# Optimization experiments

Hardware: AMD Instinct MI355X
Metric: run time of the kernel (lower is better)

## Reference

```python
import jax, jax.numpy as jnp
import numpy as np

N = 131072
C = 8
W = 256


def setup_inputs() -> dict:
    key = jax.random.key(0)
    ks = jax.random.split(key, 10)
    s1 = 1.0 / np.sqrt(3.0)
    sw = 1.0 / np.sqrt(W)
    return {
        "positions": jax.random.normal(ks[0], (N, 3), dtype=jnp.float32),
        "times": jax.random.randint(ks[1], (N,), 0, C, dtype=jnp.int64),
        "W1": jax.random.normal(ks[2], (C, 3, W), dtype=jnp.float32) * s1,
        "b1": jnp.zeros((C, W), dtype=jnp.float32),
        "W2": jax.random.normal(ks[3], (C, W, W), dtype=jnp.float32) * sw,
        "b2": jnp.zeros((C, W), dtype=jnp.float32),
        "W3": jax.random.normal(ks[4], (C, W, W), dtype=jnp.float32) * sw,
        "b3": jnp.zeros((C, W), dtype=jnp.float32),
        "W4": jax.random.normal(ks[5], (C, W, 3), dtype=jnp.float32) * sw,
        "b4": jnp.zeros((C, 3), dtype=jnp.float32),
    }


def _mlp(x, w1, c1, w2, c2, w3, c3, w4, c4):
    # 4-layer MLP, Tanh hidden activations and Tanh output activation
    h = jnp.tanh(x @ w1 + c1)
    h = jnp.tanh(h @ w2 + c2)
    h = jnp.tanh(h @ w3 + c3)
    return jnp.tanh(h @ w4 + c4)


def reference(positions, times, W1, b1, W2, b2, W3, b3, W4, b4):
    # offsets = zeros_like(positions); offsets[times==i] = mlp_i(positions[times==i])
    # classes partition the points, so this equals a per-class select-sum.
    offsets = jnp.zeros_like(positions)
    for i in range(C):  # small fixed class count
        out_i = _mlp(positions, W1[i], b1[i], W2[i], b2[i], W3[i], b3[i], W4[i], b4[i])
        mask = (times == i)[:, None]  # [N,1]
        offsets = jnp.where(mask, out_i, offsets)
    return offsets
```

## Files before the change

kernel.cpp:

```cpp
#include <hip/hip_runtime.h>
#include <stdint.h>

#define N_PTS 131072
#define NCLS 8
#define MT 64
#define CAP 32768
#define PS 2.8853900817779268f

typedef __bf16 bf16x8 __attribute__((ext_vector_type(8)));
typedef float f32x4 __attribute__((ext_vector_type(4)));

__device__ __forceinline__ float exp2_fast(float a) {
#if __has_builtin(__builtin_amdgcn_exp2f)
  return __builtin_amdgcn_exp2f(a);
#else
  return exp2f(a);
#endif
}

__device__ __forceinline__ float tanh_p2(float a) {
  return fmaf(-2.0f, __builtin_amdgcn_rcpf(exp2_fast(a) + 1.0f), 1.0f);
}

__device__ __forceinline__ unsigned short f2bf_rne(float f) {
  unsigned u = __float_as_uint(f);
  u = u + 0x7fffu + ((u >> 16) & 1u);
  return (unsigned short)(u >> 16);
}

__device__ __forceinline__ unsigned pack_bf16(float a, float b) {
  unsigned ua = __float_as_uint(a) + 0x8000u;
  unsigned ub = __float_as_uint(b) + 0x8000u;
  return __builtin_amdgcn_perm(ub, ua, 0x07060302u);
}

#define PK2_BLKS 512
#define MISC_BLKS 177
#define MISC_N 45184
#define SCAT_BLKS 512
#define PREP_GRID (PK2_BLKS + MISC_BLKS + SCAT_BLKS)

__global__ __launch_bounds__(256) void k_prep(
    const int* __restrict__ times,
    const float* __restrict__ W1, const float* __restrict__ b1,
    const float* __restrict__ W2, const float* __restrict__ b2,
    const float* __restrict__ W3, const float* __restrict__ b3,
    const float* __restrict__ W4, const float* __restrict__ b4,
    int* __restrict__ hdr, int* __restrict__ sortedIdx,
    unsigned short* __restrict__ packed23,
    float* __restrict__ w1p, float* __restrict__ b2p,
    float* __restrict__ b3p, float* __restrict__ b4p,
    unsigned short* __restrict__ W4p) {
  __shared__ int lh[NCLS], lbase[NCLS];

  int b = blockIdx.x;
  int tid = threadIdx.x;

  if (b < PK2_BLKS) {
    int cl = b >> 5;
    int k8 = b & 31;
    int j = tid;
    int l = cl >> 3, c = cl & 7;
    const float* W = (l ? W3 : W2) + c * 65536 + k8 * 8 * 256 + j;
    float v0 = W[0],        v1 = W[256],     v2 = W[2 * 256], v3 = W[3 * 256];
    float v4 = W[4 * 256],  v5 = W[5 * 256], v6 = W[6 * 256], v7 = W[7 * 256];
    uint4 pk;
    pk.x = (unsigned)f2bf_rne(PS * v0) | ((unsigned)f2bf_rne(PS * v1) << 16);
    pk.y = (unsigned)f2bf_rne(PS * v2) | ((unsigned)f2bf_rne(PS * v3) << 16);
    pk.z = (unsigned)f2bf_rne(PS * v4) | ((unsigned)f2bf_rne(PS * v5) << 16);
    pk.w = (unsigned)f2bf_rne(PS * v6) | ((unsigned)f2bf_rne(PS * v7) << 16);
    *(uint4*)&packed23[cl * 65536 + (k8 * 256 + j) * 8] = pk;
  } else if (b < PK2_BLKS + MISC_BLKS) {
    int e2 = (b - PK2_BLKS) * 256 + tid;
    if (e2 < 8192) {
      int c = e2 >> 10, rem = e2 & 1023;
      int j = rem >> 2, t = rem & 3;
      float v = (t < 3) ? W1[c * 768 + t * 256 + j] : b1[c * 256 + j];
      w1p[e2] = PS * v;
    } else if (e2 < 10240) {
      int i = e2 - 8192;
      b2p[i] = PS * b2[i];
    } else if (e2 < 12288) {
      int i = e2 - 10240;
      b3p[i] = PS * b3[i];
    } else if (e2 < 12416) {
      int i = e2 - 12288;
      int c = i >> 4, r = i & 15;
      b4p[i] = (r < 3) ? PS * b4[c * 3 + r] : 0.0f;
    } else if (e2 < MISC_N) {
      int i = e2 - 12416;
      int c = i >> 12, rem = i & 4095;
      int jj = rem & 7, j = (rem >> 3) & 15, k = ((rem >> 7) << 3) + jj;
      float v = (j < 3) ? PS * W4[c * 768 + k * 3 + j] : 0.0f;
      W4p[c * 4096 + rem] = f2bf_rne(v);
    }
  } else {
    int sb = b - (PK2_BLKS + MISC_BLKS);
    if (tid < NCLS) lh[tid] = 0;
    __syncthreads();
    int i = sb * 256 + tid;
    int t = times[i];
    int r = atomicAdd(&lh[t], 1);
    __syncthreads();
    if (tid < NCLS) lbase[tid] = lh[tid] ? atomicAdd(&hdr[tid], lh[tid]) : 0;
    __syncthreads();
    sortedIdx[t * CAP + lbase[t] + r] = i;
  }
}

template <bool PRELOAD_NEXT>
__device__ __forceinline__ void mfma_layer16(
    unsigned short (*__restrict__ Abuf)[MT][8],
    bf16x8 (&af)[2][8],
    bf16x8 (&afn)[2][8],
    const bf16x8* __restrict__ nextAf,
    const float* __restrict__ biasp,
    int tid) {
  int lane = tid & 63, w = tid >> 6;
  int quad = lane >> 4, l16 = lane & 15;
  int jcol = w * 32 + l16;

  f32x4 acc[2][4];
#pragma unroll
  for (int jf = 0; jf < 2; jf++) {
    f32x4 bv = *(const f32x4*)&biasp[w * 32 + jf * 16 + quad * 4];
#pragma unroll
    for (int mt = 0; mt < 4; mt++) acc[jf][mt] = bv;
  }

#pragma unroll
  for (int kb = 0; kb < 8; kb++) {
    int kq = kb * 4 + quad;
    bf16x8 bfr[4];
#pragma unroll
    for (int mt = 0; mt < 4; mt++)
      bfr[mt] = *(const bf16x8*)&Abuf[kq][mt * 16 + l16][0];
#pragma unroll
    for (int jf = 0; jf < 2; jf++)
#pragma unroll
      for (int mt = 0; mt < 4; mt++)
        acc[jf][mt] = __builtin_amdgcn_mfma_f32_16x16x32_bf16(af[jf][kb], bfr[mt], acc[jf][mt], 0, 0, 0);
  }

  __syncthreads();

  if (PRELOAD_NEXT) {
#pragma unroll
    for (int jf = 0; jf < 2; jf++)
#pragma unroll
      for (int kb = 0; kb < 8; kb++)
        afn[jf][kb] = nextAf[(kb * 4 + quad) * 256 + jcol + jf * 16];
  }

#pragma unroll
  for (int jf = 0; jf < 2; jf++) {
    int jbase = w * 32 + jf * 16 + quad * 4;
#pragma unroll
    for (int mt = 0; mt < 4; mt++) {
      float t0 = tanh_p2(acc[jf][mt][0]);
      float t1 = tanh_p2(acc[jf][mt][1]);
      float t2 = tanh_p2(acc[jf][mt][2]);
      float t3 = tanh_p2(acc[jf][mt][3]);
      uint2 pk = make_uint2(pack_bf16(t0, t1), pack_bf16(t2, t3));
      *(uint2*)&Abuf[jbase >> 3][mt * 16 + l16][jbase & 7] = pk;
    }
  }
}

__global__ __launch_bounds__(512, 4) void k_mlp(
    const float* __restrict__ pos,
    const int* __restrict__ hdr, const int* __restrict__ sortedIdx,
    const unsigned short* __restrict__ packed23,
    const float* __restrict__ w1p, const float* __restrict__ b2p,
    const float* __restrict__ b3p, const float* __restrict__ b4p,
    const unsigned short* __restrict__ W4p,
    float* __restrict__ out) {

  __shared__ __align__(16) unsigned short Abuf[32][MT][8];
  __shared__ __align__(16) float4 w1i[256];
  __shared__ __align__(16) float4 xpos4[MT];
  __shared__ int sIdx[MT];

  int b = blockIdx.x;
  int tid = threadIdx.x;

  int c = -1, t0 = 0, cnt = 0;
  {
    int ts = 0;
#pragma unroll
    for (int cc = 0; cc < NCLS; cc++) {
      int cc_cnt = hdr[cc];
      int tiles = (cc_cnt + MT - 1) >> 6;
      if (b >= ts && b < ts + tiles) { c = cc; t0 = b - ts; cnt = cc_cnt; }
      ts += tiles;
    }
  }
  if (c < 0) return;
  int base = c * CAP + t0 * MT;
  int mCount = min(MT, cnt - t0 * MT);

  int lane = tid & 63, w = tid >> 6;
  int quad = lane >> 4, l16 = lane & 15;
  int jcol = w * 32 + l16;

  const bf16x8* Af2 = (const bf16x8*)(packed23 + ((size_t)c << 16));
  const bf16x8* Af3 = (const bf16x8*)(packed23 + ((size_t)(8 + c) << 16));
  bf16x8 afA[2][8], afB[2][8];
#pragma unroll
  for (int jf = 0; jf < 2; jf++)
#pragma unroll
    for (int kb = 0; kb < 8; kb++)
      afA[jf][kb] = Af2[(kb * 4 + quad) * 256 + jcol + jf * 16];

  if (tid < MT) sIdx[tid] = sortedIdx[base + min(tid, mCount - 1)];
  if (tid < 256) w1i[tid] = ((const float4*)(w1p + (size_t)c * 1024))[tid];
  __syncthreads();
  if (tid < MT) {
    int idx = sIdx[tid] * 3;
    xpos4[tid] = make_float4(pos[idx], pos[idx + 1], pos[idx + 2], 0.0f);
  }
  __syncthreads();

  {
    int m = tid & 63, q = tid >> 6;
    float4 xp = xpos4[m];
#pragma unroll
    for (int i8 = 0; i8 < 4; i8++) {
      int j8 = q * 4 + i8;
      unsigned pk[4];
#pragma unroll
      for (int jp = 0; jp < 4; jp++) {
        float t[2];
#pragma unroll
        for (int u = 0; u < 2; u++) {
          float4 wv = w1i[j8 * 8 + jp * 2 + u];
          float a = fmaf(xp.x, wv.x, fmaf(xp.y, wv.y, fmaf(xp.z, wv.z, wv.w)));
          t[u] = tanh_p2(a);
        }
        pk[jp] = pack_bf16(t[0], t[1]);
      }
      *(uint4*)&Abuf[j8][m][0] = make_uint4(pk[0], pk[1], pk[2], pk[3]);
    }
  }
  __syncthreads();

  mfma_layer16<true>(Abuf, afA, afB, Af3, b2p + c * 256, tid);
  __syncthreads();
  mfma_layer16<false>(Abuf, afB, afA, nullptr, b3p + c * 256, tid);
  __syncthreads();

  if (w < 4) {
    f32x4 acc = *(const f32x4*)&b4p[c * 16 + quad * 4];
#pragma unroll
    for (int kb = 0; kb < 8; kb++) {
      int kq = kb * 4 + quad;
      bf16x8 a4 = *(const bf16x8*)&W4p[((size_t)c * 512 + kq * 16 + l16) * 8];
      bf16x8 b4f = *(const bf16x8*)&Abuf[kq][w * 16 + l16][0];
      acc = __builtin_amdgcn_mfma_f32_16x16x32_bf16(a4, b4f, acc, 0, 0, 0);
    }
    int m = w * 16 + l16;
    if (quad == 0 && m < mCount) {
      int o = sIdx[m] * 3;
      out[o + 0] = tanh_p2(acc[0]);
      out[o + 1] = tanh_p2(acc[1]);
      out[o + 2] = tanh_p2(acc[2]);
    }
  }
}

extern "C" void kernel_launch(void* const* d_in, const int* in_sizes, int n_in,
                              void* d_out, int out_size, void* d_ws, size_t ws_size,
                              hipStream_t stream) {
  const float* pos = (const float*)d_in[0];
  const int* times = (const int*)d_in[1];
  const float* W1 = (const float*)d_in[2];
  const float* b1 = (const float*)d_in[3];
  const float* W2 = (const float*)d_in[4];
  const float* b2 = (const float*)d_in[5];
  const float* W3 = (const float*)d_in[6];
  const float* b3 = (const float*)d_in[7];
  const float* W4 = (const float*)d_in[8];
  const float* b4 = (const float*)d_in[9];

  char* ws = (char*)d_ws;
  int* hdr = (int*)ws;
  int* sortedIdx = (int*)(ws + 4096);
  float* w1p = (float*)(ws + 1052672);
  float* b2p = (float*)(ws + 1085440);
  float* b3p = (float*)(ws + 1093632);
  float* b4p = (float*)(ws + 1101824);
  unsigned short* W4p = (unsigned short*)(ws + 1102336);
  unsigned short* packed23 = (unsigned short*)(ws + (2u << 20));
  float* out = (float*)d_out;

  hipMemsetAsync(d_ws, 0, 64, stream);
  k_prep<<<PREP_GRID, 256, 0, stream>>>(times, W1, b1, W2, b2, W3, b3, W4, b4,
                                        hdr, sortedIdx, packed23,
                                        w1p, b2p, b3p, b4p, W4p);
  k_mlp<<<N_PTS / MT + NCLS, 512, 0, stream>>>(
      pos, hdr, sortedIdx, packed23, w1p, b2p, b3p, b4p, W4p, out);
}
```

Measured before the change: 140.3 us.

## Halve MLP block to 256 threads with 64 output columns per wave, drop weight preload

The MLP kernel now runs with 4 waves per block instead of 8. Each wave computes 64 output columns (4 column fragments) per layer instead of 32. Weight fragments are loaded from global memory inside the k-loop rather than preloaded into registers, including the previous layer-3 prefetch that overlapped the tanh epilogue. This cuts block size and register-held weights to raise occupancy and remove the idle waves in the final layer. In exchange, each wave does twice the MFMA work and the weight load latency is now exposed inside the main loop.

```diff
diff --git a/kernel.cpp b/kernel.cpp
--- a/kernel.cpp
+++ b/kernel.cpp
@@ -108,22 +108,19 @@
   }
 }
 
-template <bool PRELOAD_NEXT>
 __device__ __forceinline__ void mfma_layer16(
     unsigned short (*__restrict__ Abuf)[MT][8],
-    bf16x8 (&af)[2][8],
-    bf16x8 (&afn)[2][8],
-    const bf16x8* __restrict__ nextAf,
+    const bf16x8* __restrict__ Af,
     const float* __restrict__ biasp,
     int tid) {
   int lane = tid & 63, w = tid >> 6;
   int quad = lane >> 4, l16 = lane & 15;
-  int jcol = w * 32 + l16;
-
-  f32x4 acc[2][4];
-#pragma unroll
-  for (int jf = 0; jf < 2; jf++) {
-    f32x4 bv = *(const f32x4*)&biasp[w * 32 + jf * 16 + quad * 4];
+  int jbase = w * 64;
+
+  f32x4 acc[4][4];
+#pragma unroll
+  for (int jf = 0; jf < 4; jf++) {
+    f32x4 bv = *(const f32x4*)&biasp[jbase + jf * 16 + quad * 4];
 #pragma unroll
     for (int mt = 0; mt < 4; mt++) acc[jf][mt] = bv;
   }
@@ -131,30 +128,25 @@
 #pragma unroll
   for (int kb = 0; kb < 8; kb++) {
     int kq = kb * 4 + quad;
-    bf16x8 bfr[4];
+    bf16x8 af[4], bfr[4];
+#pragma unroll
+    for (int jf = 0; jf < 4; jf++)
+      af[jf] = Af[kq * 256 + jbase + jf * 16 + l16];
 #pragma unroll
     for (int mt = 0; mt < 4; mt++)
       bfr[mt] = *(const bf16x8*)&Abuf[kq][mt * 16 + l16][0];
 #pragma unroll
-    for (int jf = 0; jf < 2; jf++)
+    for (int jf = 0; jf < 4; jf++)
 #pragma unroll
       for (int mt = 0; mt < 4; mt++)
-        acc[jf][mt] = __builtin_amdgcn_mfma_f32_16x16x32_bf16(af[jf][kb], bfr[mt], acc[jf][mt], 0, 0, 0);
-  }
-
-  __syncthreads();
-
-  if (PRELOAD_NEXT) {
-#pragma unroll
-    for (int jf = 0; jf < 2; jf++)
-#pragma unroll
-      for (int kb = 0; kb < 8; kb++)
-        afn[jf][kb] = nextAf[(kb * 4 + quad) * 256 + jcol + jf * 16];
-  }
-
-#pragma unroll
-  for (int jf = 0; jf < 2; jf++) {
-    int jbase = w * 32 + jf * 16 + quad * 4;
+        acc[jf][mt] = __builtin_amdgcn_mfma_f32_16x16x32_bf16(af[jf], bfr[mt], acc[jf][mt], 0, 0, 0);
+  }
+
+  __syncthreads();
+
+#pragma unroll
+  for (int jf = 0; jf < 4; jf++) {
+    int jbq = jbase + jf * 16 + quad * 4;
 #pragma unroll
     for (int mt = 0; mt < 4; mt++) {
       float t0 = tanh_p2(acc[jf][mt][0]);
@@ -162,12 +154,12 @@
       float t2 = tanh_p2(acc[jf][mt][2]);
       float t3 = tanh_p2(acc[jf][mt][3]);
       uint2 pk = make_uint2(pack_bf16(t0, t1), pack_bf16(t2, t3));
-      *(uint2*)&Abuf[jbase >> 3][mt * 16 + l16][jbase & 7] = pk;
-    }
-  }
-}
-
-__global__ __launch_bounds__(512, 4) void k_mlp(
+      *(uint2*)&Abuf[jbq >> 3][mt * 16 + l16][jbq & 7] = pk;
+    }
+  }
+}
+
+__global__ __launch_bounds__(256, 4) void k_mlp(
     const float* __restrict__ pos,
     const int* __restrict__ hdr, const int* __restrict__ sortedIdx,
     const unsigned short* __restrict__ packed23,
@@ -199,21 +191,8 @@
   int base = c * CAP + t0 * MT;
   int mCount = min(MT, cnt - t0 * MT);
 
-  int lane = tid & 63, w = tid >> 6;
-  int quad = lane >> 4, l16 = lane & 15;
-  int jcol = w * 32 + l16;
-
-  const bf16x8* Af2 = (const bf16x8*)(packed23 + ((size_t)c << 16));
-  const bf16x8* Af3 = (const bf16x8*)(packed23 + ((size_t)(8 + c) << 16));
-  bf16x8 afA[2][8], afB[2][8];
-#pragma unroll
-  for (int jf = 0; jf < 2; jf++)
-#pragma unroll
-    for (int kb = 0; kb < 8; kb++)
-      afA[jf][kb] = Af2[(kb * 4 + quad) * 256 + jcol + jf * 16];
-
   if (tid < MT) sIdx[tid] = sortedIdx[base + min(tid, mCount - 1)];
-  if (tid < 256) w1i[tid] = ((const float4*)(w1p + (size_t)c * 1024))[tid];
+  w1i[tid] = ((const float4*)(w1p + (size_t)c * 1024))[tid];
   __syncthreads();
   if (tid < MT) {
     int idx = sIdx[tid] * 3;
@@ -225,8 +204,8 @@
     int m = tid & 63, q = tid >> 6;
     float4 xp = xpos4[m];
 #pragma unroll
-    for (int i8 = 0; i8 < 4; i8++) {
-      int j8 = q * 4 + i8;
+    for (int i8 = 0; i8 < 8; i8++) {
+      int j8 = q * 8 + i8;
       unsigned pk[4];
 #pragma unroll
       for (int jp = 0; jp < 4; jp++) {
@@ -244,12 +223,16 @@
   }
   __syncthreads();
 
-  mfma_layer16<true>(Abuf, afA, afB, Af3, b2p + c * 256, tid);
-  __syncthreads();
-  mfma_layer16<false>(Abuf, afB, afA, nullptr, b3p + c * 256, tid);
-  __syncthreads();
-
-  if (w < 4) {
+  mfma_layer16(Abuf, (const bf16x8*)(packed23 + ((size_t)c << 16)),
+               b2p + c * 256, tid);
+  __syncthreads();
+  mfma_layer16(Abuf, (const bf16x8*)(packed23 + ((size_t)(8 + c) << 16)),
+               b3p + c * 256, tid);
+  __syncthreads();
+
+  {
+    int lane = tid & 63, w = tid >> 6;
+    int quad = lane >> 4, l16 = lane & 15;
     f32x4 acc = *(const f32x4*)&b4p[c * 16 + quad * 4];
 #pragma unroll
     for (int kb = 0; kb < 8; kb++) {
@@ -297,6 +280,6 @@
   k_prep<<<PREP_GRID, 256, 0, stream>>>(times, W1, b1, W2, b2, W3, b3, W4, b4,
                                         hdr, sortedIdx, packed23,
                                         w1p, b2p, b3p, b4p, W4p);
-  k_mlp<<<N_PTS / MT + NCLS, 512, 0, stream>>>(
+  k_mlp<<<N_PTS / MT + NCLS, 256, 0, stream>>>(
       pos, hdr, sortedIdx, packed23, w1p, b2p, b3p, b4p, W4p, out);
 }
```

New measurement: 131.9 us. 6.0% less time.
